# Performance work log

Measured on AMD Instinct MI355X. Metric: run time of the kernel, lower is better.

The kernel has to match this reference:

```python
import jax, jax.numpy as jnp
import numpy as np

B, C, H, W = 4, 64, 224, 224
MAX_SEG = 256       # max superpixel label -> segment buffer size 257
MAX_SEG_REF = 256


def _superfeatures(feat, labels, num_seg):
    """scatter_max segment pooling over interior pixels.
    feat [B,C,H,W], labels [B,1,H,W] int -> [B,C,num_seg]."""
    b, c = feat.shape[:2]
    src = feat[:, :, 1:-1, 1:-1].reshape(b, c, -1)   # [B,C,P]
    idx = labels[:, 0, 1:-1, 1:-1].reshape(b, -1)    # [B,P]

    def one(s, i):
        m = jax.ops.segment_max(s.T, i, num_segments=num_seg)  # [S,C]
        return jnp.where(jnp.isneginf(m), 0.0, m).T            # empty segments -> 0

    return jax.vmap(one)(src, idx)                   # [B,C,S]


def _chan_norm(x, eps=1e-5):
    # per-superpixel: subtract channel mean, divide by channel L2 norm (torch dim=1)
    xm = x - jnp.mean(x, axis=1, keepdims=True)
    return xm / (jnp.linalg.norm(xm, axis=1, keepdims=True) + eps)


def setup_inputs():
    key = jax.random.key(0)
    ks = jax.random.split(key, 11)
    rn = lambda k, sh: jax.random.normal(k, sh, dtype=jnp.float32)
    return {
        "feat_target": rn(ks[0], (B, C, H, W)),
        "feat_ref": rn(ks[1], (B, C, H, W)),
        "feat_rgb_ref": rn(ks[2], (B, C, H, W)),
        "Wq": rn(ks[3], (C, C)) * 0.1, "bq": rn(ks[4], (C,)) * 0.1,
        "Wk": rn(ks[5], (C, C)) * 0.1, "bk": rn(ks[6], (C,)) * 0.1,
        "Wv": rn(ks[7], (C, C)) * 0.1, "bv": rn(ks[8], (C,)) * 0.1,
        "label_mask_target": jax.random.randint(ks[9], (B, 1, H, W), 0, MAX_SEG + 1, dtype=jnp.int32),
        "label_mask_ref": jax.random.randint(ks[10], (B, 1, H, W), 0, MAX_SEG_REF + 1, dtype=jnp.int32),
        "max_segments": MAX_SEG,
        "max_segments_ref": MAX_SEG_REF,
    }


def reference(feat_target, feat_ref, feat_rgb_ref, Wq, bq, Wk, bk, Wv, bv,
              label_mask_target, label_mask_ref, max_segments, max_segments_ref):
    S_t = max_segments + 1
    S_r = max_segments_ref + 1
    b, c, h, w = feat_target.shape

    # Superfeatures: segment pooling (scatter_max)
    enc_t = _superfeatures(feat_target, label_mask_target, S_t)   # [B,C,S_t]
    enc_r = _superfeatures(feat_ref, label_mask_ref, S_r)         # [B,C,S_r]
    enc_v = _superfeatures(feat_rgb_ref, label_mask_ref, S_r)     # [B,C,S_r]

    # per-sample variable lengths (label_target / label_ref in the torch loop)
    n_t = jnp.max(label_mask_target.reshape(b, -1), axis=1) + 1
    n_r = jnp.max(label_mask_ref.reshape(b, -1), axis=1) + 1
    tmask = jnp.arange(S_t)[None, :] < n_t[:, None]               # [B,S_t]
    rmask = jnp.arange(S_r)[None, :] < n_r[:, None]               # [B,S_r]

    # Superattention_conv (batched over the original per-sample loop)
    q = jnp.einsum('oc,bcn->bon', Wq, _chan_norm(enc_t)) + bq[None, :, None]
    k = jnp.einsum('oc,bcm->bom', Wk, _chan_norm(enc_r)) + bk[None, :, None]
    v = jnp.einsum('oc,bcm->bom', Wv, enc_v) + bv[None, :, None]  # value conv on raw rgb feats

    sim = jnp.einsum('bcn,bcm->bnm', q, k) / 0.01                 # temperature 0.01
    sim = jnp.where(rmask[:, None, :], sim, -jnp.inf)             # mask invalid ref cols
    attn = jax.nn.softmax(sim, axis=2) * tmask[:, :, None]        # softmax dim=2, zero pad rows

    wg = jnp.einsum('bnm,bcm->bcn', attn, v)                      # [B,C,S_t] (transposed wg_ref)

    # Unpool_features: gather back to pixel grid
    idx = jnp.broadcast_to(label_mask_target.reshape(b, 1, -1), (b, c, h * w))
    unpool = jnp.take_along_axis(wg, idx, axis=2).reshape(b, c, h, w)
    return unpool
```

## Files before the change

kernel.cpp:

```cpp
#include <hip/hip_runtime.h>
#include <math.h>

#define BB 4
#define CC 64
#define HH 224
#define WW 224
#define HWW (HH*WW)
#define SS 257
#define CPB 8
#define NRC 8
#define RPC 28
#define ENCW (3*BB*CC*SS)

__device__ __forceinline__ unsigned fkey(float f) {
    unsigned u = __float_as_uint(f);
    return (u & 0x80000000u) ? ~u : (u | 0x80000000u);
}
__device__ __forceinline__ float funkey(unsigned k) {
    return (k & 0x80000000u) ? __uint_as_float(k & 0x7FFFFFFFu) : __uint_as_float(~k);
}
#define SENT 0x007FFFFFu

__global__ __launch_bounds__(256) void init_kernel(unsigned* __restrict__ enc,
                                                   int* __restrict__ nmax) {
    int i = blockIdx.x * 256 + threadIdx.x;
    if (i < ENCW / 4) ((uint4*)enc)[i] = make_uint4(SENT, SENT, SENT, SENT);
    if (i < 2 * BB) nmax[i] = 0;
}

__global__ __launch_bounds__(256, 3) void pool_kernel(
    const float* __restrict__ fT, const float* __restrict__ fR,
    const float* __restrict__ fV,
    const int* __restrict__ labT, const int* __restrict__ labR,
    unsigned* __restrict__ enc, int* __restrict__ nmax)
{
    __shared__ unsigned seg[CPB * SS];
    __shared__ int wmax[4];
    const int cg = blockIdx.x, rc = blockIdx.y;
    const int z = blockIdx.z >> 2, b = blockIdx.z & 3;
    const float* src = (z == 0) ? fT : (z == 1) ? fR : fV;
    const int*   lab = (z == 0) ? labT : labR;

    for (int i = threadIdx.x; i < CPB * SS; i += 256) seg[i] = SENT;
    __syncthreads();

    const int h0 = rc * RPC;
    const int*    lp  = lab + (size_t)b * HWW;
    const int4*   lp4 = (const int4*)lp;
    const float4* fp4 = (const float4*)(src + (size_t)(b * CC + cg * CPB) * HWW);
    const int PS4 = HWW / 4;

    const bool do_nmax = (cg == 0) && (z < 2);
    int lmax = -1;

    #pragma unroll
    for (int it = 0; it < (RPC * 56 + 255) / 256; ++it) {
        int gi = min(it * 256 + (int)threadIdx.x, RPC * 56 - 1);
        int h = gi / 56;
        int g = gi - h * 56;
        int hi = min(h0 + h + 1, 222);
        int idx4 = hi * 56 + g;
        int4   l = lp4[idx4];
        float4 f[CPB];
        #pragma unroll
        for (int j = 0; j < CPB; ++j) f[j] = fp4[idx4 + j * PS4];
        __builtin_amdgcn_sched_barrier(0);

        if (do_nmax)
            lmax = max(lmax, max(max(l.x, l.y), max(l.z, l.w)));
        const bool mx = (g != 0), mw = (g != 55);
        #pragma unroll
        for (int j = 0; j < CPB; ++j) {
            unsigned kx = fkey(f[j].x), ky = fkey(f[j].y);
            unsigned kz = fkey(f[j].z), kw = fkey(f[j].w);
            unsigned* sg = seg + j * SS;
            if (mx && kx > sg[l.x]) atomicMax(&sg[l.x], kx);
            if (ky > sg[l.y]) atomicMax(&sg[l.y], ky);
            if (kz > sg[l.z]) atomicMax(&sg[l.z], kz);
            if (mw && kw > sg[l.w]) atomicMax(&sg[l.w], kw);
        }
    }

    if (do_nmax && threadIdx.x < 56) {
        if (rc == 0) {
            int4 l = lp4[threadIdx.x];
            lmax = max(lmax, max(max(l.x, l.y), max(l.z, l.w)));
        }
        if (rc == NRC - 1) {
            int4 l = lp4[223 * 56 + threadIdx.x];
            lmax = max(lmax, max(max(l.x, l.y), max(l.z, l.w)));
        }
    }
    #pragma unroll
    for (int o = 32; o; o >>= 1) lmax = max(lmax, __shfl_xor(lmax, o, 64));
    if ((threadIdx.x & 63) == 0) wmax[threadIdx.x >> 6] = lmax;
    __syncthreads();
    if (do_nmax && threadIdx.x == 0) {
        int m = max(max(wmax[0], wmax[1]), max(wmax[2], wmax[3]));
        atomicMax(&nmax[z * BB + b], m + 1);
    }

    unsigned* gp = enc + (size_t)((z * BB + b) * CC + cg * CPB) * SS;
    for (int i = threadIdx.x; i < CPB * SS; i += 256) {
        unsigned k = seg[i];
        if (k != SENT) atomicMax(&gp[i], k);
    }
}

__global__ __launch_bounds__(512) void qkv_kernel(
    const unsigned* __restrict__ enc,
    const float* __restrict__ Wq, const float* __restrict__ bq,
    const float* __restrict__ Wk, const float* __restrict__ bk,
    const float* __restrict__ Wv, const float* __restrict__ bv,
    float* __restrict__ qkv)
{
    const int z = blockIdx.z, b = blockIdx.y;
    const int wid = threadIdx.x >> 6, lane = threadIdx.x & 63;
    const int n = blockIdx.x * 8 + wid;
    if (n >= SS) return;

    const float* Wm = (z == 0) ? Wq : (z == 1) ? Wk : Wv;
    const float* bm = (z == 0) ? bq : (z == 1) ? bk : bv;
    const unsigned* ep = enc + (size_t)((z * BB + b) * CC) * SS + n;

    unsigned kraw = ep[(size_t)lane * SS];
    float x = (kraw == SENT) ? 0.0f : funkey(kraw);
    if (z != 2) {
        float s = x;
        for (int o = 32; o; o >>= 1) s += __shfl_xor(s, o, 64);
        float xm = x - s * (1.0f / 64.0f);
        float s2 = xm * xm;
        for (int o = 32; o; o >>= 1) s2 += __shfl_xor(s2, o, 64);
        x = xm / (sqrtf(s2) + 1e-5f);
    }
    float acc = bm[lane];
    #pragma unroll
    for (int cI = 0; cI < 64; ++cI) {
        float xc = __shfl(x, cI, 64);
        acc = fmaf(Wm[lane * 64 + cI], xc, acc);
    }
    qkv[(size_t)((z * BB + b) * SS + n) * CC + lane] = acc;
}

__global__ __launch_bounds__(256) void attn_kernel(
    const float* __restrict__ qkv, const int* __restrict__ nmax,
    float* __restrict__ wg)
{
    const int n = blockIdx.x, b = blockIdx.y, t = threadIdx.x;
    __shared__ float qs[CC];
    __shared__ float sim[512];
    __shared__ float red[256];
    __shared__ float pv[4][64];

    const int nT = nmax[b], nR = nmax[BB + b];
    float* wp = wg + (size_t)(b * SS + n) * CC;
    if (n >= nT) {
        if (t < CC) wp[t] = 0.0f;
        return;
    }
    const float* q = qkv + (size_t)(0 * BB + b) * SS * CC;
    const float* k = qkv + (size_t)(1 * BB + b) * SS * CC;
    const float* v = qkv + (size_t)(2 * BB + b) * SS * CC;

    if (t < CC) qs[t] = q[(size_t)n * CC + t];
    sim[t] = -INFINITY;
    sim[t + 256] = -INFINITY;
    __syncthreads();

    for (int m = t; m < SS; m += 256) {
        float s = -INFINITY;
        if (m < nR) {
            const float4* kr = (const float4*)(k + (size_t)m * CC);
            float acc = 0.0f;
            #pragma unroll
            for (int i = 0; i < 16; ++i) {
                float4 kv = kr[i];
                acc += qs[4*i+0]*kv.x + qs[4*i+1]*kv.y + qs[4*i+2]*kv.z + qs[4*i+3]*kv.w;
            }
            s = acc * 100.0f;
        }
        sim[m] = s;
    }
    __syncthreads();

    red[t] = fmaxf(sim[t], sim[t + 256]);
    __syncthreads();
    for (int s = 128; s > 0; s >>= 1) {
        if (t < s) red[t] = fmaxf(red[t], red[t + s]);
        __syncthreads();
    }
    const float mx = red[0];
    __syncthreads();

    float psum = 0.0f;
    for (int m = t; m < SS; m += 256) {
        float e = expf(sim[m] - mx);
        sim[m] = e;
        psum += e;
    }
    red[t] = psum;
    __syncthreads();
    for (int s = 128; s > 0; s >>= 1) {
        if (t < s) red[t] += red[t + s];
        __syncthreads();
    }
    const float rdenom = 1.0f / red[0];

    const int g = t >> 6, c = t & 63;
    float acc = 0.0f;
    for (int m = g; m < SS; m += 4)
        acc = fmaf(sim[m], v[(size_t)m * CC + c], acc);
    pv[g][c] = acc;
    __syncthreads();
    if (t < CC)
        wp[t] = (pv[0][t] + pv[1][t] + pv[2][t] + pv[3][t]) * rdenom;
}

__global__ __launch_bounds__(256) void unpool_kernel(
    const float* __restrict__ wg, const int* __restrict__ labT,
    float* __restrict__ out)
{
    const int idx = blockIdx.x * 256 + threadIdx.x;
    if (idx >= BB * HWW) return;
    const int b = idx / HWW, hw = idx - b * HWW;
    const int l = labT[idx];
    const float4* row = (const float4*)(wg + (size_t)(b * SS + l) * CC);
    float* op = out + (size_t)b * CC * HWW + hw;
    #pragma unroll
    for (int i = 0; i < 16; ++i) {
        float4 r = row[i];
        op[(size_t)(4*i+0) * HWW] = r.x;
        op[(size_t)(4*i+1) * HWW] = r.y;
        op[(size_t)(4*i+2) * HWW] = r.z;
        op[(size_t)(4*i+3) * HWW] = r.w;
    }
}

extern "C" void kernel_launch(void* const* d_in, const int* in_sizes, int n_in,
                              void* d_out, int out_size, void* d_ws, size_t ws_size,
                              hipStream_t stream) {
    (void)in_sizes; (void)n_in; (void)out_size; (void)ws_size;
    const float* fT  = (const float*)d_in[0];
    const float* fR  = (const float*)d_in[1];
    const float* fV  = (const float*)d_in[2];
    const float* Wq  = (const float*)d_in[3];
    const float* bq  = (const float*)d_in[4];
    const float* Wk  = (const float*)d_in[5];
    const float* bk  = (const float*)d_in[6];
    const float* Wv  = (const float*)d_in[7];
    const float* bv  = (const float*)d_in[8];
    const int* labT  = (const int*)d_in[9];
    const int* labR  = (const int*)d_in[10];
    float* out = (float*)d_out;

    unsigned* enc = (unsigned*)d_ws;
    float* qkv  = (float*)d_ws + ENCW;
    float* wg   = qkv + 3 * BB * CC * SS;
    int*   nmax = (int*)(wg + BB * CC * SS);

    init_kernel<<<(ENCW / 4 + 255) / 256, 256, 0, stream>>>(enc, nmax);
    pool_kernel<<<dim3(CPB, NRC, 12), 256, 0, stream>>>(fT, fR, fV, labT, labR, enc, nmax);
    qkv_kernel<<<dim3((SS + 7) / 8, BB, 3), 512, 0, stream>>>(enc, Wq, bq, Wk, bk, Wv, bv, qkv);
    attn_kernel<<<dim3(SS, BB), 256, 0, stream>>>(qkv, nmax, wg);
    unpool_kernel<<<(BB * HWW + 255) / 256, 256, 0, stream>>>(wg, labT, out);
}
```

Baseline: 91.82 us.

## Double-buffer pool loads into LDS via global_load_lds and re-tile grid

The segment-max pooling kernel now streams label and feature tiles straight into shared memory with async global-to-LDS loads, double-buffered with explicit vmcnt waits. This is meant to overlap memory fetch with the LDS atomic-max work. The grid is re-tiled to 4 channels per block and 7 chunks of 32 rows, which gives 16x7x12 blocks instead of 8x8x12. Border rows are now masked per pixel rather than clamped, and the separate border-row nmax pass is dropped because every row is now loaded. In exchange it uses more LDS per block and relies on hand-written waitcnt ordering.

Measured after the change: 93.73 us. +2.1%, slower.

```diff
diff --git a/kernel.cpp b/kernel.cpp
--- a/kernel.cpp
+++ b/kernel.cpp
@@ -7,9 +7,9 @@
 #define WW 224
 #define HWW (HH*WW)
 #define SS 257
-#define CPB 8
-#define NRC 8
-#define RPC 28
+#define CPB 4
+#define NCHK 7
+#define NSTEP 7
 #define ENCW (3*BB*CC*SS)
 
 __device__ __forceinline__ unsigned fkey(float f) {
@@ -20,6 +20,12 @@
     return (k & 0x80000000u) ? __uint_as_float(k & 0x7FFFFFFFu) : __uint_as_float(~k);
 }
 #define SENT 0x007FFFFFu
+
+__device__ __forceinline__ void gll16(const void* g, void* l) {
+    __builtin_amdgcn_global_load_lds(
+        (const __attribute__((address_space(1))) unsigned*)g,
+        (__attribute__((address_space(3))) unsigned*)l, 16, 0, 0);
+}
 
 __global__ __launch_bounds__(256) void init_kernel(unsigned* __restrict__ enc,
                                                    int* __restrict__ nmax) {
@@ -28,80 +34,92 @@
     if (i < 2 * BB) nmax[i] = 0;
 }
 
-__global__ __launch_bounds__(256, 3) void pool_kernel(
+__global__ __launch_bounds__(256) void pool_kernel(
     const float* __restrict__ fT, const float* __restrict__ fR,
     const float* __restrict__ fV,
     const int* __restrict__ labT, const int* __restrict__ labR,
     unsigned* __restrict__ enc, int* __restrict__ nmax)
 {
+    __shared__ float4   fbuf[2][CPB][256];
+    __shared__ int4     lbuf[2][256];
     __shared__ unsigned seg[CPB * SS];
-    __shared__ int wmax[4];
-    const int cg = blockIdx.x, rc = blockIdx.y;
+    __shared__ int      wmax[4];
+
+    const int cg = blockIdx.x, chunk = blockIdx.y;
     const int z = blockIdx.z >> 2, b = blockIdx.z & 3;
     const float* src = (z == 0) ? fT : (z == 1) ? fR : fV;
     const int*   lab = (z == 0) ? labT : labR;
-
-    for (int i = threadIdx.x; i < CPB * SS; i += 256) seg[i] = SENT;
-    __syncthreads();
-
-    const int h0 = rc * RPC;
-    const int*    lp  = lab + (size_t)b * HWW;
-    const int4*   lp4 = (const int4*)lp;
+    const int t = threadIdx.x;
+    const int wbase = t & ~63;
+
+    for (int i = t; i < CPB * SS; i += 256) seg[i] = SENT;
+    __syncthreads();
+
+    const int g0 = chunk * (32 * 56);
+    const int4*   lp4 = (const int4*)(lab + (size_t)b * HWW);
     const float4* fp4 = (const float4*)(src + (size_t)(b * CC + cg * CPB) * HWW);
     const int PS4 = HWW / 4;
 
     const bool do_nmax = (cg == 0) && (z < 2);
     int lmax = -1;
 
-    #pragma unroll
-    for (int it = 0; it < (RPC * 56 + 255) / 256; ++it) {
-        int gi = min(it * 256 + (int)threadIdx.x, RPC * 56 - 1);
-        int h = gi / 56;
-        int g = gi - h * 56;
-        int hi = min(h0 + h + 1, 222);
-        int idx4 = hi * 56 + g;
-        int4   l = lp4[idx4];
-        float4 f[CPB];
-        #pragma unroll
-        for (int j = 0; j < CPB; ++j) f[j] = fp4[idx4 + j * PS4];
-        __builtin_amdgcn_sched_barrier(0);
-
+    {
+        int g = g0 + t;
+        gll16(&lp4[g],            &lbuf[0][wbase]);
+        gll16(&fp4[g + 0 * PS4],  &fbuf[0][0][wbase]);
+        gll16(&fp4[g + 1 * PS4],  &fbuf[0][1][wbase]);
+        gll16(&fp4[g + 2 * PS4],  &fbuf[0][2][wbase]);
+        gll16(&fp4[g + 3 * PS4],  &fbuf[0][3][wbase]);
+    }
+
+    for (int s = 0; s < NSTEP; ++s) {
+        const int p = s & 1;
+        if (s + 1 < NSTEP) {
+            int g = g0 + (s + 1) * 256 + t;
+            gll16(&lp4[g],            &lbuf[p ^ 1][wbase]);
+            gll16(&fp4[g + 0 * PS4],  &fbuf[p ^ 1][0][wbase]);
+            gll16(&fp4[g + 1 * PS4],  &fbuf[p ^ 1][1][wbase]);
+            gll16(&fp4[g + 2 * PS4],  &fbuf[p ^ 1][2][wbase]);
+            gll16(&fp4[g + 3 * PS4],  &fbuf[p ^ 1][3][wbase]);
+            asm volatile("s_waitcnt vmcnt(5)" ::: "memory");
+        } else {
+            asm volatile("s_waitcnt vmcnt(0)" ::: "memory");
+        }
+
+        int4 l = lbuf[p][t];
         if (do_nmax)
             lmax = max(lmax, max(max(l.x, l.y), max(l.z, l.w)));
-        const bool mx = (g != 0), mw = (g != 55);
+
+        int G  = s * 256 + t;
+        int H  = chunk * 32 + G / 56;
+        int go = G % 56;
+        bool rowok = (H >= 1) && (H <= 222);
+        bool mx = rowok && (go != 0);
+        bool mw = rowok && (go != 55);
         #pragma unroll
         for (int j = 0; j < CPB; ++j) {
-            unsigned kx = fkey(f[j].x), ky = fkey(f[j].y);
-            unsigned kz = fkey(f[j].z), kw = fkey(f[j].w);
+            float4 f = fbuf[p][j][t];
+            unsigned kx = fkey(f.x), ky = fkey(f.y);
+            unsigned kz = fkey(f.z), kw = fkey(f.w);
             unsigned* sg = seg + j * SS;
-            if (mx && kx > sg[l.x]) atomicMax(&sg[l.x], kx);
-            if (ky > sg[l.y]) atomicMax(&sg[l.y], ky);
-            if (kz > sg[l.z]) atomicMax(&sg[l.z], kz);
-            if (mw && kw > sg[l.w]) atomicMax(&sg[l.w], kw);
+            if (mx    && kx > sg[l.x]) atomicMax(&sg[l.x], kx);
+            if (rowok && ky > sg[l.y]) atomicMax(&sg[l.y], ky);
+            if (rowok && kz > sg[l.z]) atomicMax(&sg[l.z], kz);
+            if (mw    && kw > sg[l.w]) atomicMax(&sg[l.w], kw);
         }
     }
 
-    if (do_nmax && threadIdx.x < 56) {
-        if (rc == 0) {
-            int4 l = lp4[threadIdx.x];
-            lmax = max(lmax, max(max(l.x, l.y), max(l.z, l.w)));
-        }
-        if (rc == NRC - 1) {
-            int4 l = lp4[223 * 56 + threadIdx.x];
-            lmax = max(lmax, max(max(l.x, l.y), max(l.z, l.w)));
-        }
-    }
     #pragma unroll
     for (int o = 32; o; o >>= 1) lmax = max(lmax, __shfl_xor(lmax, o, 64));
-    if ((threadIdx.x & 63) == 0) wmax[threadIdx.x >> 6] = lmax;
-    __syncthreads();
-    if (do_nmax && threadIdx.x == 0) {
+    if ((t & 63) == 0) wmax[t >> 6] = lmax;
+    __syncthreads();
+    if (do_nmax && t == 0) {
         int m = max(max(wmax[0], wmax[1]), max(wmax[2], wmax[3]));
         atomicMax(&nmax[z * BB + b], m + 1);
     }
 
     unsigned* gp = enc + (size_t)((z * BB + b) * CC + cg * CPB) * SS;
-    for (int i = threadIdx.x; i < CPB * SS; i += 256) {
+    for (int i = t; i < CPB * SS; i += 256) {
         unsigned k = seg[i];
         if (k != SENT) atomicMax(&gp[i], k);
     }
@@ -259,7 +277,7 @@
     int*   nmax = (int*)(wg + BB * CC * SS);
 
     init_kernel<<<(ENCW / 4 + 255) / 256, 256, 0, stream>>>(enc, nmax);
-    pool_kernel<<<dim3(CPB, NRC, 12), 256, 0, stream>>>(fT, fR, fV, labT, labR, enc, nmax);
+    pool_kernel<<<dim3(16, NCHK, 12), 256, 0, stream>>>(fT, fR, fV, labT, labR, enc, nmax);
     qkv_kernel<<<dim3((SS + 7) / 8, BB, 3), 512, 0, stream>>>(enc, Wq, bq, Wk, bk, Wv, bv, qkv);
     attn_kernel<<<dim3(SS, BB), 256, 0, stream>>>(qkv, nmax, wg);
     unpool_kernel<<<(BB * HWW + 255) / 256, 256, 0, stream>>>(wg, labT, out);
```
